# Kernel optimization log

Measured on AMD Instinct MI355X. Metric: run time of the kernel, lower is better.

The kernel has to match this reference:

```python
import jax, jax.numpy as jnp
import numpy as np
from jax import lax

B, T, H, IN = 1024, 100, 512, 4  # batch, seq len (fixed 100 in source), hidden, nucleotide dim


def _lstm_cell(x, h, c, Wih, Whh, b):
    # PyTorch gate order: i, f, g, o ; b = b_ih + b_hh
    gates = x @ Wih.T + h @ Whh.T + b
    i, f, g, o = jnp.split(gates, 4, axis=-1)
    c = jax.nn.sigmoid(f) * c + jax.nn.sigmoid(i) * jnp.tanh(g)
    h = jax.nn.sigmoid(o) * jnp.tanh(c)
    return h, c


def _run_layer(xs, Wih, Whh, b):
    # xs: [T, B, in] -> ys: [T, B, H], final (h, c)
    Bn = xs.shape[1]
    h0 = jnp.zeros((Bn, H), xs.dtype)
    c0 = jnp.zeros((Bn, H), xs.dtype)

    def step(carry, x):
        h, c = carry
        h, c = _lstm_cell(x, h, c, Wih, Whh, b)
        return (h, c), h

    (h, c), ys = lax.scan(step, (h0, c0), xs)
    return ys, h, c


def setup_inputs() -> dict:
    key = jax.random.key(0)
    ks = jax.random.split(key, 16)
    s = lambda fan: 1.0 / np.sqrt(fan)

    def W(k, shape, fan):
        return jax.random.uniform(k, shape, jnp.float32, -s(fan), s(fan))

    inp = {
        "X": jax.random.normal(ks[0], (B, T, IN), jnp.float32),
        "epoch": 10,
        # encoder LSTM (2 layers)
        "enc_Wih0": W(ks[1], (4 * H, IN), H),
        "enc_Whh0": W(ks[2], (4 * H, H), H),
        "enc_b0": jnp.zeros((4 * H,), jnp.float32),
        "enc_Wih1": W(ks[3], (4 * H, H), H),
        "enc_Whh1": W(ks[4], (4 * H, H), H),
        "enc_b1": jnp.zeros((4 * H,), jnp.float32),
        # decoder LSTM (2 layers, input dim = seq_in_dim = 4)
        "dec_Wih0": W(ks[5], (4 * H, IN), H),
        "dec_Whh0": W(ks[6], (4 * H, H), H),
        "dec_b0": jnp.zeros((4 * H,), jnp.float32),
        "dec_Wih1": W(ks[7], (4 * H, H), H),
        "dec_Whh1": W(ks[8], (4 * H, H), H),
        "dec_b1": jnp.zeros((4 * H,), jnp.float32),
        # predict_MLP = Linear(H, 4)
        "Wp": W(ks[9], (IN, H), H),
        "bp": jnp.zeros((IN,), jnp.float32),
    }
    return inp


def reference(X, epoch, enc_Wih0, enc_Whh0, enc_b0, enc_Wih1, enc_Whh1, enc_b1,
              dec_Wih0, dec_Whh0, dec_b0, dec_Wih1, dec_Whh1, dec_b1, Wp, bp):
    # ---- Encoder: 2-layer LSTM over X (batch_first -> scan over time) ----
    xs = jnp.swapaxes(X, 0, 1)  # [T, B, 4]
    ys0, h0e, c0e = _run_layer(xs, enc_Wih0, enc_Whh0, enc_b0)
    _, h1e, c1e = _run_layer(ys0, enc_Wih1, enc_Whh1, enc_b1)

    #      discretize_input=False) ----
    Bn = X.shape[0]
    x_init = jnp.zeros((Bn, IN), X.dtype)

    def dec_step(carry, _):
        x, h0, c0, h1, c1 = carry
        h0, c0 = _lstm_cell(x, h0, c0, dec_Wih0, dec_Whh0, dec_b0)
        h1, c1 = _lstm_cell(h0, h1, c1, dec_Wih1, dec_Whh1, dec_b1)
        pred = h1 @ Wp.T + bp                 # [B, 4] logits
        x_next = jax.nn.softmax(pred, axis=-1)
        return (x_next, h0, c0, h1, c1), pred

    _, preds = lax.scan(dec_step, (x_init, h0e, c0e, h1e, c1e), None, length=T)
    # out_seq list of [B,1,4] in torch -> stacked [B, 100, 4]
    return jnp.swapaxes(preds, 0, 1)
```

## Files before the change

kernel.cpp:

```cpp
#include <hip/hip_runtime.h>
#include <math.h>
#include <stdint.h>

typedef _Float16 f16;
typedef _Float16 f16x8 __attribute__((ext_vector_type(8)));
typedef float f32x16 __attribute__((ext_vector_type(16)));

#define BATCH 1024
#define HD    512
#define TST   100

__device__ __forceinline__ float4 coh_ld_x4(const void* p) {
    float4 v;
    asm volatile("global_load_dwordx4 %0, %1, off sc0 sc1" : "=v"(v) : "v"(p) : "memory");
    return v;
}
__device__ __forceinline__ float4 ld_x4(const void* p) {
    float4 v;
    asm volatile("global_load_dwordx4 %0, %1, off" : "=v"(v) : "v"(p) : "memory");
    return v;
}
__device__ __forceinline__ void coh_store_u32(uint32_t* p, uint32_t v) {
    asm volatile("global_store_dword %0, %1, off sc0 sc1" :: "v"(p), "v"(v) : "memory");
}
__device__ __forceinline__ void coh_store_i32(int* p, int v) {
    asm volatile("global_store_dword %0, %1, off sc0 sc1" :: "v"(p), "v"(v) : "memory");
}
__device__ __forceinline__ int coh_load_i32(const int* p) {
    int v;
    asm volatile("global_load_dword %0, %1, off sc0 sc1\n\ts_waitcnt vmcnt(0)"
                 : "=v"(v) : "v"(p) : "memory");
    return v;
}
__device__ __forceinline__ void drain_vm() {
    asm volatile("s_waitcnt vmcnt(0)" ::: "memory");
    __builtin_amdgcn_sched_barrier(0);
}
__device__ __forceinline__ void wait_vm(int n) {
    switch (n) {
    case 0:  asm volatile("s_waitcnt vmcnt(0)"  ::: "memory"); break;
    case 4:  asm volatile("s_waitcnt vmcnt(4)"  ::: "memory"); break;
    case 6:  asm volatile("s_waitcnt vmcnt(6)"  ::: "memory"); break;
    case 10: asm volatile("s_waitcnt vmcnt(10)" ::: "memory"); break;
    case 26: asm volatile("s_waitcnt vmcnt(26)" ::: "memory"); break;
    case 32: asm volatile("s_waitcnt vmcnt(32)" ::: "memory"); break;
    default: asm volatile("s_waitcnt vmcnt(34)" ::: "memory"); break;
    }
    __builtin_amdgcn_sched_barrier(0);
}

__device__ __forceinline__ float fast_sig(float x) {
    return 1.0f / (1.0f + __expf(-x));
}
__device__ __forceinline__ float fast_tanh(float x) {
    float xc = fminf(fmaxf(x, -15.0f), 15.0f);
    float e = __expf(2.0f * xc);
    return 1.0f - 2.0f / (e + 1.0f);
}

__global__ void split_w(const float* __restrict__ src0, int ksplit,
                        const float* __restrict__ src1, int NKT, f16* __restrict__ out)
{
    int c = blockIdx.x * 256 + threadIdx.x;
    int total = 8 * NKT * 4096;
    if (c >= total) return;
    int q = c & 4095;
    int t2 = c >> 12;
    int kt = t2 % NKT;
    int mt = t2 / NKT;
    int inner = q >> 8;
    int row = q & 255;
    int s = inner >> 2, p = (inner >> 1) & 1, half = inner & 1;
    int m = mt * 256 + row;
    int orow = (m & 3) * HD + (m >> 2);
    int kb = kt * 64 + s * 16 + half * 8;
    f16 v[8];
    #pragma unroll
    for (int e = 0; e < 8; ++e) {
        int k = kb + e;
        float w = (k < ksplit) ? src0[(size_t)orow * ksplit + k]
                               : src1[(size_t)orow * HD + (k - ksplit)];
        float w32 = w * 32.0f;
        f16 hi = (f16)w32;
        v[e] = p ? (f16)((w32 - (float)hi) * 2048.0f) : hi;
    }
    *(f16x8*)(out + (size_t)c * 8) = *(f16x8*)v;
}

__global__ void prep_b4(const float* __restrict__ b, float* __restrict__ bt) {
    int c = blockIdx.x * 256 + threadIdx.x;
    if (c < 2048) bt[c] = b[(c & 3) * HD + (c >> 2)];
}

__global__ void prep_wih4(const float* __restrict__ W, float* __restrict__ o) {
    int c = blockIdx.x * 256 + threadIdx.x;
    if (c < 8192) {
        int j = c & 3, g = (c >> 2) & 3, hl = c >> 4;
        o[c] = W[(size_t)(g * HD + hl) * 4 + j];
    }
}

__device__ __forceinline__ void publish(int* cell, int epoch) {
    drain_vm();
    __syncthreads();
    if (threadIdx.x == 0)
        coh_store_i32(cell, epoch);
}

__device__ __forceinline__ void wait2(const int* a, int ta, const int* b, int tb) {
    if (threadIdx.x < 64) {
        const int l = threadIdx.x & 7;
        const bool useB = (threadIdx.x & 8) != 0;
        const int* p = (useB ? b : a) + l * 16;
        const int tgt = useB ? tb : ta;
        for (;;) {
            int v = coh_load_i32(p);
            if (__all(v >= tgt)) break;
            __builtin_amdgcn_s_sleep(2);
        }
    }
    __syncthreads();
}

template<int NKT, bool RANK4>
__device__ __forceinline__ void layer_step(
    const f16* __restrict__ Wst, const f16* __restrict__ src1, const f16* __restrict__ src2,
    const float* __restrict__ wih4, const float* __restrict__ xin, int xstride,
    const float* __restrict__ bt4, float* __restrict__ cT, f16* __restrict__ hout,
    char* smem, int mt, int nt)
{
    const int tid  = threadIdx.x;
    const int lane = tid & 63;
    const int wv   = tid >> 6;
    const int col  = lane & 31;
    const int half = lane >> 5;
    const int xk   = lane & 15;
    const int n0   = nt * 32;

    const size_t tbaseA = (size_t)half * 4096 + (size_t)(wv * 64 + col) * 16;
    const int colb = col * 256;

    float4 ab0[4], ab1[4], ab2[4], ab3[4];
    float4 rb0[2], rb1[2];
    float4 xv = make_float4(0.f, 0.f, 0.f, 0.f);

    auto issueA = [&](int kt, int s, float4 (&bank)[4]) {
        const char* ga = (const char*)Wst + ((size_t)(mt * NKT + kt) << 16)
                       + ((size_t)s << 14) + tbaseA;
        bank[0] = ld_x4(ga);
        bank[1] = ld_x4(ga + 8192);
        bank[2] = ld_x4(ga + 512);
        bank[3] = ld_x4(ga + 8704);
    };
    auto issueB = [&](int kt, float4 (&rb)[2]) {
        #pragma unroll
        for (int i = 0; i < 2; ++i) {
            int u = i * 256 + tid;
            int bc = u >> 4, w16 = u & 15;
            int si = w16 ^ (bc & 15);
            int p = si >> 3;
            int kh = kt * 64 + ((si >> 1) & 3) * 16 + (si & 1) * 8;
            const f16* sp = src1; int kl = kh;
            if (NKT == 16 && kh >= 512) { sp = src2; kl = kh - 512; }
            rb[i] = coh_ld_x4(sp + (size_t)(n0 + bc) * 1024 + p * 512 + kl);
        }
    };

    f32x16 accA0 = {}, accA1 = {}, accB0 = {}, accB1 = {};

    if (RANK4) xv = coh_ld_x4(xin + (size_t)(n0 + col) * xstride);
    issueB(0, rb0);
    issueB(1, rb1);
    issueA(0, 0, ab0);
    issueA(0, 1, ab1);

    #pragma unroll
    for (int kt = 0; kt < NKT; ++kt) {
        char* buf = smem + (kt & 1) * 8192;
        wait_vm(kt == 0 ? 10 : kt == 1 ? 26 : kt == NKT - 1 ? 32 : 34);
        if ((kt & 1) == 0) {
            *(float4*)(buf + tid * 16)        = rb0[0];
            *(float4*)(buf + 4096 + tid * 16) = rb0[1];
            if (kt + 2 < NKT) issueB(kt + 2, rb0);
        } else {
            *(float4*)(buf + tid * 16)        = rb1[0];
            *(float4*)(buf + 4096 + tid * 16) = rb1[1];
            if (kt + 2 < NKT) issueB(kt + 2, rb1);
        }
        __syncthreads();

        #define KSTEP(S, BK)                                                              \
        {                                                                                 \
            f16x8 bh = *(const f16x8*)(buf + colb + ((((S) * 2 + half) ^ xk) << 4));       \
            f16x8 bl = *(const f16x8*)(buf + colb + (((8 + (S) * 2 + half) ^ xk) << 4));   \
            f16x8 ah0 = __builtin_bit_cast(f16x8, BK[0]);                                 \
            f16x8 al0 = __builtin_bit_cast(f16x8, BK[1]);                                 \
            f16x8 ah1 = __builtin_bit_cast(f16x8, BK[2]);                                 \
            f16x8 al1 = __builtin_bit_cast(f16x8, BK[3]);                                 \
            accA0 = __builtin_amdgcn_mfma_f32_32x32x16_f16(ah0, bh, accA0, 0, 0, 0);      \
            accB0 = __builtin_amdgcn_mfma_f32_32x32x16_f16(al0, bh, accB0, 0, 0, 0);      \
            accB0 = __builtin_amdgcn_mfma_f32_32x32x16_f16(ah0, bl, accB0, 0, 0, 0);      \
            accA1 = __builtin_amdgcn_mfma_f32_32x32x16_f16(ah1, bh, accA1, 0, 0, 0);      \
            accB1 = __builtin_amdgcn_mfma_f32_32x32x16_f16(al1, bh, accB1, 0, 0, 0);      \
            accB1 = __builtin_amdgcn_mfma_f32_32x32x16_f16(ah1, bl, accB1, 0, 0, 0);      \
        }

        wait_vm(kt >= NKT - 2 ? 4 : 6);
        KSTEP(0, ab0)
        issueA(kt, 2, ab2);
        wait_vm(kt >= NKT - 2 ? 4 : 6);
        KSTEP(1, ab1)
        issueA(kt, 3, ab3);
        wait_vm(4);
        KSTEP(2, ab2)
        if (kt + 1 < NKT) issueA(kt + 1, 0, ab0);
        wait_vm(kt == NKT - 1 ? 0 : 4);
        KSTEP(3, ab3)
        if (kt + 1 < NKT) issueA(kt + 1, 1, ab1);
        #undef KSTEP
    }

    const float sA = 1.0f / 1024.0f;
    const float sB = 1.0f / (1024.0f * 2048.0f);
    uint32_t* htile = (uint32_t*)(smem + 16384);

    #pragma unroll
    for (int f = 0; f < 2; ++f) {
        const f32x16 aA = f ? accA1 : accA0;
        const f32x16 aB = f ? accB1 : accB0;
        #pragma unroll
        for (int qq = 0; qq < 4; ++qq) {
            const int hl_loc = wv * 16 + f * 8 + 2 * qq + half;
            const int hl = mt * 64 + hl_loc;
            const float4 bv = *(const float4*)(bt4 + hl * 4);
            float g0 = aA[4 * qq + 0] * sA + aB[4 * qq + 0] * sB + bv.x;
            float g1 = aA[4 * qq + 1] * sA + aB[4 * qq + 1] * sB + bv.y;
            float g2 = aA[4 * qq + 2] * sA + aB[4 * qq + 2] * sB + bv.z;
            float g3 = aA[4 * qq + 3] * sA + aB[4 * qq + 3] * sB + bv.w;
            if (RANK4) {
                const float4* wr = (const float4*)(wih4 + hl * 16);
                g0 += wr[0].x * xv.x + wr[0].y * xv.y + wr[0].z * xv.z + wr[0].w * xv.w;
                g1 += wr[1].x * xv.x + wr[1].y * xv.y + wr[1].z * xv.z + wr[1].w * xv.w;
                g2 += wr[2].x * xv.x + wr[2].y * xv.y + wr[2].z * xv.z + wr[2].w * xv.w;
                g3 += wr[3].x * xv.x + wr[3].y * xv.y + wr[3].z * xv.z + wr[3].w * xv.w;
            }
            const int n = n0 + col;
            const size_t co = (size_t)hl * 1024 + n;
            const float cold = cT[co];
            const float si = fast_sig(g0);
            const float sf = fast_sig(g1);
            const float so = fast_sig(g3);
            const float cn = sf * cold + si * fast_tanh(g2);
            const float hn = so * fast_tanh(cn);
            cT[co] = cn;
            const float h32v = hn * 32.0f;
            const f16 hi = (f16)h32v;
            const f16 lo = (f16)((h32v - (float)hi) * 2048.0f);
            uint32_t pk = ((uint32_t)__builtin_bit_cast(uint16_t, lo) << 16)
                        | (uint32_t)__builtin_bit_cast(uint16_t, hi);
            htile[col * 65 + hl_loc] = pk;
        }
    }
    __syncthreads();
    uint32_t* h32out = (uint32_t*)hout;
    #pragma unroll
    for (int e = 0; e < 8; ++e) {
        int u = e * 256 + tid;
        int cc = u >> 6;
        int rem = u & 63;
        int pl = rem >> 5;
        int w = rem & 31;
        uint32_t t0 = htile[cc * 65 + 2 * w];
        uint32_t t1 = htile[cc * 65 + 2 * w + 1];
        uint32_t word = pl ? ((t1 & 0xffff0000u) | (t0 >> 16))
                           : ((t1 << 16) | (t0 & 0xffffu));
        coh_store_u32(h32out + (size_t)(n0 + cc) * 512 + pl * 256 + mt * 32 + w, word);
    }
}

__device__ __forceinline__ void pred_step(
    const f16* __restrict__ h1, const float* __restrict__ Wp, const float* __restrict__ bp,
    float* __restrict__ outp, float* __restrict__ xfb, int t, int mt, int nt)
{
    const int lane = threadIdx.x & 63;
    const int wv = threadIdx.x >> 6;
    const int n = nt * 32 + mt * 4 + wv;
    const f16* hr = h1 + (size_t)n * 1024;
    const int k0 = lane * 8;
    float4 hv4 = coh_ld_x4(hr + k0);
    float4 lv4 = coh_ld_x4(hr + 512 + k0);
    drain_vm();
    f16x8 hv = __builtin_bit_cast(f16x8, hv4);
    f16x8 lv = __builtin_bit_cast(f16x8, lv4);
    float h[8];
    #pragma unroll
    for (int e = 0; e < 8; ++e)
        h[e] = (float)hv[e] * 0.03125f + (float)lv[e] * (1.0f / 65536.0f);
    float a[4] = {};
    #pragma unroll
    for (int g = 0; g < 4; ++g) {
        const float4 wa = *(const float4*)(Wp + g * HD + k0);
        const float4 wb = *(const float4*)(Wp + g * HD + k0 + 4);
        a[g] = h[0]*wa.x + h[1]*wa.y + h[2]*wa.z + h[3]*wa.w
             + h[4]*wb.x + h[5]*wb.y + h[6]*wb.z + h[7]*wb.w;
    }
    #pragma unroll
    for (int off = 32; off > 0; off >>= 1) {
        a[0] += __shfl_xor(a[0], off);
        a[1] += __shfl_xor(a[1], off);
        a[2] += __shfl_xor(a[2], off);
        a[3] += __shfl_xor(a[3], off);
    }
    if (lane == 0) {
        const float4 bv = *(const float4*)bp;
        float v0 = a[0] + bv.x, v1 = a[1] + bv.y, v2 = a[2] + bv.z, v3 = a[3] + bv.w;
        float* op = outp + (size_t)n * (TST * 4) + t * 4;
        op[0] = v0; op[1] = v1; op[2] = v2; op[3] = v3;
        float m = fmaxf(fmaxf(v0, v1), fmaxf(v2, v3));
        float e0 = expf(v0 - m), e1 = expf(v1 - m), e2 = expf(v2 - m), e3 = expf(v3 - m);
        float inv = 1.0f / (e0 + e1 + e2 + e3);
        uint32_t* xp = (uint32_t*)(xfb + n * 4);
        float s0 = e0 * inv, s1 = e1 * inv, s2 = e2 * inv, s3 = e3 * inv;
        coh_store_u32(xp + 0, __builtin_bit_cast(uint32_t, s0));
        coh_store_u32(xp + 1, __builtin_bit_cast(uint32_t, s1));
        coh_store_u32(xp + 2, __builtin_bit_cast(uint32_t, s2));
        coh_store_u32(xp + 3, __builtin_bit_cast(uint32_t, s3));
    }
}

struct Params {
    const f16 *WE0, *WE1, *WD0, *WD1;
    const float *wih4E, *wih4D, *btE0, *btE1, *btD0, *btD1;
    const float *X, *Wp, *bp;
    f16 *h0a, *h0b, *h1a, *h1b;
    float *c0, *c1;
    float *xfb0, *xfb1;
    float *out;
    int *f0, *f1, *fp;
};

__launch_bounds__(256, 1) __global__ void lstm_persistent(Params P)
{
    __shared__ __align__(16) char smem[16384 + 8448];
    const int bx = blockIdx.x;
    const int mt = bx & 7;
    const int nt = bx >> 3;
    int* f0g = P.f0 + nt * 128;
    int* f1g = P.f1 + nt * 128;
    int* fpg = P.fp + nt * 128;
    int* my0 = f0g + mt * 16;
    int* my1 = f1g + mt * 16;
    int* myp = fpg + mt * 16;
    f16* h0b_[2] = { P.h0a, P.h0b };
    f16* h1b_[2] = { P.h1a, P.h1b };
    float* xfb_[2] = { P.xfb0, P.xfb1 };

    for (int u = 0; u < 2 * TST; ++u) {
        const bool enc = (u < TST);
        const int t = enc ? u : u - TST;

        if (enc) wait2(f0g, u, f0g, u);
        else     wait2(f0g, u, fpg, t);
        layer_step<8, true>(enc ? P.WE0 : P.WD0,
                            h0b_[(u + 1) & 1], nullptr,
                            enc ? P.wih4E : P.wih4D,
                            enc ? (P.X + t * 4) : xfb_[(t + 1) & 1],
                            enc ? (TST * 4) : 4,
                            enc ? P.btE0 : P.btD0,
                            P.c0, h0b_[u & 1], smem, mt, nt);
        publish(my0, u + 1);

        wait2(f0g, u + 1, f1g, u);
        layer_step<16, false>(enc ? P.WE1 : P.WD1,
                              h0b_[u & 1], h1b_[(u + 1) & 1],
                              nullptr, nullptr, 0,
                              enc ? P.btE1 : P.btD1,
                              P.c1, h1b_[u & 1], smem, mt, nt);
        publish(my1, u + 1);

        if (!enc) {
            wait2(f1g, u + 1, f1g, u + 1);
            pred_step(h1b_[u & 1], P.Wp, P.bp, P.out, xfb_[t & 1], t, mt, nt);
            publish(myp, t + 1);
        }
    }
}

extern "C" void kernel_launch(void* const* d_in, const int* in_sizes, int n_in,
                              void* d_out, int out_size, void* d_ws, size_t ws_size,
                              hipStream_t stream)
{
    const float* X     = (const float*)d_in[0];
    const float* eWih0 = (const float*)d_in[2];
    const float* eWhh0 = (const float*)d_in[3];
    const float* eb0   = (const float*)d_in[4];
    const float* eWih1 = (const float*)d_in[5];
    const float* eWhh1 = (const float*)d_in[6];
    const float* eb1   = (const float*)d_in[7];
    const float* dWih0 = (const float*)d_in[8];
    const float* dWhh0 = (const float*)d_in[9];
    const float* db0   = (const float*)d_in[10];
    const float* dWih1 = (const float*)d_in[11];
    const float* dWhh1 = (const float*)d_in[12];
    const float* db1   = (const float*)d_in[13];
    const float* Wp    = (const float*)d_in[14];
    const float* bp    = (const float*)d_in[15];

    char* ws = (char*)d_ws;
    size_t off = 0;
    auto alloc = [&](size_t bytes) { char* p = ws + off; off += (bytes + 255) & ~(size_t)255; return p; };
    f16* WE0 = (f16*)alloc((size_t)8 * 8  * 65536);
    f16* WE1 = (f16*)alloc((size_t)8 * 16 * 65536);
    f16* WD0 = (f16*)alloc((size_t)8 * 8  * 65536);
    f16* WD1 = (f16*)alloc((size_t)8 * 16 * 65536);
    float* wih4E = (float*)alloc(8192 * 4);
    float* wih4D = (float*)alloc(8192 * 4);
    float* btE0 = (float*)alloc(2048 * 4);
    float* btE1 = (float*)alloc(2048 * 4);
    float* btD0 = (float*)alloc(2048 * 4);
    float* btD1 = (float*)alloc(2048 * 4);
    f16* h0a = (f16*)alloc((size_t)BATCH * 1024 * 2);
    f16* h0b = (f16*)alloc((size_t)BATCH * 1024 * 2);
    f16* h1a = (f16*)alloc((size_t)BATCH * 1024 * 2);
    f16* h1b = (f16*)alloc((size_t)BATCH * 1024 * 2);
    float* c0  = (float*)alloc((size_t)HD * BATCH * 4);
    float* c1  = (float*)alloc((size_t)HD * BATCH * 4);
    float* xfb0 = (float*)alloc((size_t)BATCH * 4 * 4);
    float* xfb1 = (float*)alloc((size_t)BATCH * 4 * 4);
    int* f0 = (int*)alloc(32 * 128 * 4);
    int* f1 = (int*)alloc(32 * 128 * 4);
    int* fp = (int*)alloc(32 * 128 * 4);
    if (off > ws_size) return;

    split_w<<<(8 * 8  * 4096) / 256, 256, 0, stream>>>(nullptr, 0,   eWhh0, 8,  WE0);
    split_w<<<(8 * 16 * 4096) / 256, 256, 0, stream>>>(eWih1, 512, eWhh1, 16, WE1);
    split_w<<<(8 * 8  * 4096) / 256, 256, 0, stream>>>(nullptr, 0,   dWhh0, 8,  WD0);
    split_w<<<(8 * 16 * 4096) / 256, 256, 0, stream>>>(dWih1, 512, dWhh1, 16, WD1);
    prep_wih4<<<32, 256, 0, stream>>>(eWih0, wih4E);
    prep_wih4<<<32, 256, 0, stream>>>(dWih0, wih4D);
    prep_b4<<<8, 256, 0, stream>>>(eb0, btE0);
    prep_b4<<<8, 256, 0, stream>>>(eb1, btE1);
    prep_b4<<<8, 256, 0, stream>>>(db0, btD0);
    prep_b4<<<8, 256, 0, stream>>>(db1, btD1);

    hipMemsetAsync(h0b, 0, (size_t)BATCH * 1024 * 2, stream);
    hipMemsetAsync(h1b, 0, (size_t)BATCH * 1024 * 2, stream);
    hipMemsetAsync(c0, 0, (size_t)HD * BATCH * 4, stream);
    hipMemsetAsync(c1, 0, (size_t)HD * BATCH * 4, stream);
    hipMemsetAsync(xfb1, 0, (size_t)BATCH * 4 * 4, stream);
    hipMemsetAsync(f0, 0, 32 * 128 * 4, stream);
    hipMemsetAsync(f1, 0, 32 * 128 * 4, stream);
    hipMemsetAsync(fp, 0, 32 * 128 * 4, stream);

    Params P;
    P.WE0 = WE0; P.WE1 = WE1; P.WD0 = WD0; P.WD1 = WD1;
    P.wih4E = wih4E; P.wih4D = wih4D;
    P.btE0 = btE0; P.btE1 = btE1; P.btD0 = btD0; P.btD1 = btD1;
    P.X = X; P.Wp = Wp; P.bp = bp;
    P.h0a = h0a; P.h0b = h0b; P.h1a = h1a; P.h1b = h1b;
    P.c0 = c0; P.c1 = c1;
    P.xfb0 = xfb0; P.xfb1 = xfb1;
    P.out = (float*)d_out;
    P.f0 = f0; P.f1 = f1; P.fp = fp;

    lstm_persistent<<<256, 256, 0, stream>>>(P);

    (void)in_sizes; (void)n_in; (void)out_size;
}
```

Baseline: 7.458 ms.

## Enlarge persistent LSTM tiles to 128 hidden units by 64 batch with 512-thread blocks

Result: slower. 17.91 ms (+140.1%).

```diff
diff --git a/kernel.cpp b/kernel.cpp
--- a/kernel.cpp
+++ b/kernel.cpp
@@ -41,10 +41,8 @@
     case 0:  asm volatile("s_waitcnt vmcnt(0)"  ::: "memory"); break;
     case 4:  asm volatile("s_waitcnt vmcnt(4)"  ::: "memory"); break;
     case 6:  asm volatile("s_waitcnt vmcnt(6)"  ::: "memory"); break;
-    case 10: asm volatile("s_waitcnt vmcnt(10)" ::: "memory"); break;
-    case 26: asm volatile("s_waitcnt vmcnt(26)" ::: "memory"); break;
-    case 32: asm volatile("s_waitcnt vmcnt(32)" ::: "memory"); break;
-    default: asm volatile("s_waitcnt vmcnt(34)" ::: "memory"); break;
+    case 8:  asm volatile("s_waitcnt vmcnt(8)"  ::: "memory"); break;
+    default: asm volatile("s_waitcnt vmcnt(10)" ::: "memory"); break;
     }
     __builtin_amdgcn_sched_barrier(0);
 }
@@ -62,16 +60,16 @@
                         const float* __restrict__ src1, int NKT, f16* __restrict__ out)
 {
     int c = blockIdx.x * 256 + threadIdx.x;
-    int total = 8 * NKT * 4096;
+    int total = 4 * NKT * 8192;
     if (c >= total) return;
-    int q = c & 4095;
-    int t2 = c >> 12;
+    int u = c & 8191;
+    int t2 = c >> 13;
     int kt = t2 % NKT;
     int mt = t2 / NKT;
-    int inner = q >> 8;
-    int row = q & 255;
+    int inner = u >> 9;
+    int row = u & 511;
     int s = inner >> 2, p = (inner >> 1) & 1, half = inner & 1;
-    int m = mt * 256 + row;
+    int m = mt * 512 + row;
     int orow = (m & 3) * HD + (m >> 2);
     int kb = kt * 64 + s * 16 + half * 8;
     f16 v[8];
@@ -106,11 +104,10 @@
     if (threadIdx.x == 0)
         coh_store_i32(cell, epoch);
 }
-
 __device__ __forceinline__ void wait2(const int* a, int ta, const int* b, int tb) {
     if (threadIdx.x < 64) {
-        const int l = threadIdx.x & 7;
-        const bool useB = (threadIdx.x & 8) != 0;
+        const int l = threadIdx.x & 3;
+        const bool useB = (threadIdx.x & 4) != 0;
         const int* p = (useB ? b : a) + l * 16;
         const int tgt = useB ? tb : ta;
         for (;;) {
@@ -134,28 +131,26 @@
     const int wv   = tid >> 6;
     const int col  = lane & 31;
     const int half = lane >> 5;
-    const int xk   = lane & 15;
-    const int n0   = nt * 32;
-
-    const size_t tbaseA = (size_t)half * 4096 + (size_t)(wv * 64 + col) * 16;
-    const int colb = col * 256;
-
-    float4 ab0[4], ab1[4], ab2[4], ab3[4];
+    const int xk   = col & 15;
+    const int n0   = nt * 64;
+
+    const size_t tbaseA = (size_t)half * 8192 + (size_t)(wv * 64 + col) * 16;
+
+    float4 abk[4][4];
     float4 rb0[2], rb1[2];
-    float4 xv = make_float4(0.f, 0.f, 0.f, 0.f);
 
     auto issueA = [&](int kt, int s, float4 (&bank)[4]) {
-        const char* ga = (const char*)Wst + ((size_t)(mt * NKT + kt) << 16)
-                       + ((size_t)s << 14) + tbaseA;
+        const char* ga = (const char*)Wst + ((size_t)(mt * NKT + kt) << 17)
+                       + ((size_t)s << 15) + tbaseA;
         bank[0] = ld_x4(ga);
-        bank[1] = ld_x4(ga + 8192);
+        bank[1] = ld_x4(ga + 16384);
         bank[2] = ld_x4(ga + 512);
-        bank[3] = ld_x4(ga + 8704);
+        bank[3] = ld_x4(ga + 16384 + 512);
     };
     auto issueB = [&](int kt, float4 (&rb)[2]) {
         #pragma unroll
         for (int i = 0; i < 2; ++i) {
-            int u = i * 256 + tid;
+            int u = i * 512 + tid;
             int bc = u >> 4, w16 = u & 15;
             int si = w16 ^ (bc & 15);
             int p = si >> 3;
@@ -166,115 +161,130 @@
         }
     };
 
-    f32x16 accA0 = {}, accA1 = {}, accB0 = {}, accB1 = {};
-
-    if (RANK4) xv = coh_ld_x4(xin + (size_t)(n0 + col) * xstride);
+    f32x16 accA[2][2] = {};
+    f32x16 accB[2][2] = {};
+
     issueB(0, rb0);
     issueB(1, rb1);
-    issueA(0, 0, ab0);
-    issueA(0, 1, ab1);
+    issueA(0, 0, abk[0]);
+    issueA(0, 1, abk[1]);
 
     #pragma unroll
     for (int kt = 0; kt < NKT; ++kt) {
-        char* buf = smem + (kt & 1) * 8192;
-        wait_vm(kt == 0 ? 10 : kt == 1 ? 26 : kt == NKT - 1 ? 32 : 34);
+        char* buf = smem + (kt & 1) * 16384;
+        wait_vm(kt == NKT - 1 ? 8 : 10);
         if ((kt & 1) == 0) {
             *(float4*)(buf + tid * 16)        = rb0[0];
-            *(float4*)(buf + 4096 + tid * 16) = rb0[1];
-            if (kt + 2 < NKT) issueB(kt + 2, rb0);
+            *(float4*)(buf + 8192 + tid * 16) = rb0[1];
         } else {
             *(float4*)(buf + tid * 16)        = rb1[0];
-            *(float4*)(buf + 4096 + tid * 16) = rb1[1];
-            if (kt + 2 < NKT) issueB(kt + 2, rb1);
+            *(float4*)(buf + 8192 + tid * 16) = rb1[1];
         }
         __syncthreads();
 
-        #define KSTEP(S, BK)                                                              \
-        {                                                                                 \
-            f16x8 bh = *(const f16x8*)(buf + colb + ((((S) * 2 + half) ^ xk) << 4));       \
-            f16x8 bl = *(const f16x8*)(buf + colb + (((8 + (S) * 2 + half) ^ xk) << 4));   \
-            f16x8 ah0 = __builtin_bit_cast(f16x8, BK[0]);                                 \
-            f16x8 al0 = __builtin_bit_cast(f16x8, BK[1]);                                 \
-            f16x8 ah1 = __builtin_bit_cast(f16x8, BK[2]);                                 \
-            f16x8 al1 = __builtin_bit_cast(f16x8, BK[3]);                                 \
-            accA0 = __builtin_amdgcn_mfma_f32_32x32x16_f16(ah0, bh, accA0, 0, 0, 0);      \
-            accB0 = __builtin_amdgcn_mfma_f32_32x32x16_f16(al0, bh, accB0, 0, 0, 0);      \
-            accB0 = __builtin_amdgcn_mfma_f32_32x32x16_f16(ah0, bl, accB0, 0, 0, 0);      \
-            accA1 = __builtin_amdgcn_mfma_f32_32x32x16_f16(ah1, bh, accA1, 0, 0, 0);      \
-            accB1 = __builtin_amdgcn_mfma_f32_32x32x16_f16(al1, bh, accB1, 0, 0, 0);      \
-            accB1 = __builtin_amdgcn_mfma_f32_32x32x16_f16(ah1, bl, accB1, 0, 0, 0);      \
-        }
-
-        wait_vm(kt >= NKT - 2 ? 4 : 6);
-        KSTEP(0, ab0)
-        issueA(kt, 2, ab2);
-        wait_vm(kt >= NKT - 2 ? 4 : 6);
-        KSTEP(1, ab1)
-        issueA(kt, 3, ab3);
+        #define KSTEP(S, BK)                                                          \
+        {                                                                             \
+            f16x8 ah0 = __builtin_bit_cast(f16x8, BK[0]);                             \
+            f16x8 al0 = __builtin_bit_cast(f16x8, BK[1]);                             \
+            f16x8 ah1 = __builtin_bit_cast(f16x8, BK[2]);                             \
+            f16x8 al1 = __builtin_bit_cast(f16x8, BK[3]);                             \
+            _Pragma("unroll")                                                         \
+            for (int nf = 0; nf < 2; ++nf) {                                          \
+                const char* cb = buf + (nf * 32 + col) * 256;                         \
+                f16x8 bh = *(const f16x8*)(cb + ((((S) * 2 + half) ^ xk) << 4));      \
+                f16x8 bl = *(const f16x8*)(cb + (((8 + (S) * 2 + half) ^ xk) << 4));  \
+                accA[0][nf] = __builtin_amdgcn_mfma_f32_32x32x16_f16(ah0, bh, accA[0][nf], 0, 0, 0); \
+                accB[0][nf] = __builtin_amdgcn_mfma_f32_32x32x16_f16(al0, bh, accB[0][nf], 0, 0, 0); \
+                accB[0][nf] = __builtin_amdgcn_mfma_f32_32x32x16_f16(ah0, bl, accB[0][nf], 0, 0, 0); \
+                accA[1][nf] = __builtin_amdgcn_mfma_f32_32x32x16_f16(ah1, bh, accA[1][nf], 0, 0, 0); \
+                accB[1][nf] = __builtin_amdgcn_mfma_f32_32x32x16_f16(al1, bh, accB[1][nf], 0, 0, 0); \
+                accB[1][nf] = __builtin_amdgcn_mfma_f32_32x32x16_f16(ah1, bl, accB[1][nf], 0, 0, 0); \
+            }                                                                         \
+        }
+
+        const int w01 = (kt == 0 || kt == NKT - 1) ? 4 : 6;
+        wait_vm(w01);
+        KSTEP(0, abk[0])
+        issueA(kt, 2, abk[2]);
+        wait_vm(w01);
+        KSTEP(1, abk[1])
+        issueA(kt, 3, abk[3]);
         wait_vm(4);
-        KSTEP(2, ab2)
-        if (kt + 1 < NKT) issueA(kt + 1, 0, ab0);
+        KSTEP(2, abk[2])
+        if (kt + 1 < NKT) issueA(kt + 1, 0, abk[0]);
         wait_vm(kt == NKT - 1 ? 0 : 4);
-        KSTEP(3, ab3)
-        if (kt + 1 < NKT) issueA(kt + 1, 1, ab1);
+        KSTEP(3, abk[3])
+        if (kt + 1 < NKT) issueA(kt + 1, 1, abk[1]);
+        if (kt + 2 < NKT) {
+            if ((kt & 1) == 0) issueB(kt + 2, rb0);
+            else               issueB(kt + 2, rb1);
+        }
         #undef KSTEP
     }
 
     const float sA = 1.0f / 1024.0f;
     const float sB = 1.0f / (1024.0f * 2048.0f);
-    uint32_t* htile = (uint32_t*)(smem + 16384);
-
+    float4 xq[2];
+    if (RANK4) {
+        xq[0] = coh_ld_x4(xin + (size_t)(n0 + col) * xstride);
+        xq[1] = coh_ld_x4(xin + (size_t)(n0 + 32 + col) * xstride);
+        drain_vm();
+    }
+    uint32_t* htile = (uint32_t*)(smem + 32768);
     #pragma unroll
     for (int f = 0; f < 2; ++f) {
-        const f32x16 aA = f ? accA1 : accA0;
-        const f32x16 aB = f ? accB1 : accB0;
         #pragma unroll
         for (int qq = 0; qq < 4; ++qq) {
             const int hl_loc = wv * 16 + f * 8 + 2 * qq + half;
-            const int hl = mt * 64 + hl_loc;
+            const int hl = mt * 128 + hl_loc;
             const float4 bv = *(const float4*)(bt4 + hl * 4);
-            float g0 = aA[4 * qq + 0] * sA + aB[4 * qq + 0] * sB + bv.x;
-            float g1 = aA[4 * qq + 1] * sA + aB[4 * qq + 1] * sB + bv.y;
-            float g2 = aA[4 * qq + 2] * sA + aB[4 * qq + 2] * sB + bv.z;
-            float g3 = aA[4 * qq + 3] * sA + aB[4 * qq + 3] * sB + bv.w;
-            if (RANK4) {
-                const float4* wr = (const float4*)(wih4 + hl * 16);
-                g0 += wr[0].x * xv.x + wr[0].y * xv.y + wr[0].z * xv.z + wr[0].w * xv.w;
-                g1 += wr[1].x * xv.x + wr[1].y * xv.y + wr[1].z * xv.z + wr[1].w * xv.w;
-                g2 += wr[2].x * xv.x + wr[2].y * xv.y + wr[2].z * xv.z + wr[2].w * xv.w;
-                g3 += wr[3].x * xv.x + wr[3].y * xv.y + wr[3].z * xv.z + wr[3].w * xv.w;
+            #pragma unroll
+            for (int nf = 0; nf < 2; ++nf) {
+                const int col_loc = nf * 32 + col;
+                const int n = n0 + col_loc;
+                float g0 = accA[f][nf][4 * qq + 0] * sA + accB[f][nf][4 * qq + 0] * sB + bv.x;
+                float g1 = accA[f][nf][4 * qq + 1] * sA + accB[f][nf][4 * qq + 1] * sB + bv.y;
+                float g2 = accA[f][nf][4 * qq + 2] * sA + accB[f][nf][4 * qq + 2] * sB + bv.z;
+                float g3 = accA[f][nf][4 * qq + 3] * sA + accB[f][nf][4 * qq + 3] * sB + bv.w;
+                if (RANK4) {
+                    const float4* wr = (const float4*)(wih4 + hl * 16);
+                    const float4 x4 = xq[nf];
+                    g0 += wr[0].x * x4.x + wr[0].y * x4.y + wr[0].z * x4.z + wr[0].w * x4.w;
+                    g1 += wr[1].x * x4.x + wr[1].y * x4.y + wr[1].z * x4.z + wr[1].w * x4.w;
+                    g2 += wr[2].x * x4.x + wr[2].y * x4.y + wr[2].z * x4.z + wr[2].w * x4.w;
+                    g3 += wr[3].x * x4.x + wr[3].y * x4.y + wr[3].z * x4.z + wr[3].w * x4.w;
+                }
+                const size_t co = (size_t)hl * 1024 + n;
+                const float cold = cT[co];
+                const float si = fast_sig(g0);
+                const float sf = fast_sig(g1);
+                const float so = fast_sig(g3);
+                const float cn = sf * cold + si * fast_tanh(g2);
+                const float hn = so * fast_tanh(cn);
+                cT[co] = cn;
+                const float h32v = hn * 32.0f;
+                const f16 hi = (f16)h32v;
+                const f16 lo = (f16)((h32v - (float)hi) * 2048.0f);
+                uint32_t pk = ((uint32_t)__builtin_bit_cast(uint16_t, lo) << 16)
+                            | (uint32_t)__builtin_bit_cast(uint16_t, hi);
+                htile[col_loc * 129 + hl_loc] = pk;
             }
-            const int n = n0 + col;
-            const size_t co = (size_t)hl * 1024 + n;
-            const float cold = cT[co];
-            const float si = fast_sig(g0);
-            const float sf = fast_sig(g1);
-            const float so = fast_sig(g3);
-            const float cn = sf * cold + si * fast_tanh(g2);
-            const float hn = so * fast_tanh(cn);
-            cT[co] = cn;
-            const float h32v = hn * 32.0f;
-            const f16 hi = (f16)h32v;
-            const f16 lo = (f16)((h32v - (float)hi) * 2048.0f);
-            uint32_t pk = ((uint32_t)__builtin_bit_cast(uint16_t, lo) << 16)
-                        | (uint32_t)__builtin_bit_cast(uint16_t, hi);
-            htile[col * 65 + hl_loc] = pk;
         }
     }
     __syncthreads();
     uint32_t* h32out = (uint32_t*)hout;
     #pragma unroll
-    for (int e = 0; e < 8; ++e) {
-        int u = e * 256 + tid;
-        int cc = u >> 6;
-        int rem = u & 63;
-        int pl = rem >> 5;
-        int w = rem & 31;
-        uint32_t t0 = htile[cc * 65 + 2 * w];
-        uint32_t t1 = htile[cc * 65 + 2 * w + 1];
+    for (int e = 0; e < 16; ++e) {
+        int u = e * 512 + tid;
+        int cc = u >> 7;
+        int rem = u & 127;
+        int pl = rem >> 6;
+        int w = rem & 63;
+        uint32_t t0 = htile[cc * 129 + 2 * w];
+        uint32_t t1 = htile[cc * 129 + 2 * w + 1];
         uint32_t word = pl ? ((t1 & 0xffff0000u) | (t0 >> 16))
                            : ((t1 << 16) | (t0 & 0xffffu));
-        coh_store_u32(h32out + (size_t)(n0 + cc) * 512 + pl * 256 + mt * 32 + w, word);
+        coh_store_u32(h32out + (size_t)(n0 + cc) * 512 + pl * 256 + mt * 64 + w, word);
     }
 }
 
@@ -284,47 +294,50 @@
 {
     const int lane = threadIdx.x & 63;
     const int wv = threadIdx.x >> 6;
-    const int n = nt * 32 + mt * 4 + wv;
-    const f16* hr = h1 + (size_t)n * 1024;
-    const int k0 = lane * 8;
-    float4 hv4 = coh_ld_x4(hr + k0);
-    float4 lv4 = coh_ld_x4(hr + 512 + k0);
-    drain_vm();
-    f16x8 hv = __builtin_bit_cast(f16x8, hv4);
-    f16x8 lv = __builtin_bit_cast(f16x8, lv4);
-    float h[8];
     #pragma unroll
-    for (int e = 0; e < 8; ++e)
-        h[e] = (float)hv[e] * 0.03125f + (float)lv[e] * (1.0f / 65536.0f);
-    float a[4] = {};
-    #pragma unroll
-    for (int g = 0; g < 4; ++g) {
-        const float4 wa = *(const float4*)(Wp + g * HD + k0);
-        const float4 wb = *(const float4*)(Wp + g * HD + k0 + 4);
-        a[g] = h[0]*wa.x + h[1]*wa.y + h[2]*wa.z + h[3]*wa.w
-             + h[4]*wb.x + h[5]*wb.y + h[6]*wb.z + h[7]*wb.w;
-    }
-    #pragma unroll
-    for (int off = 32; off > 0; off >>= 1) {
-        a[0] += __shfl_xor(a[0], off);
-        a[1] += __shfl_xor(a[1], off);
-        a[2] += __shfl_xor(a[2], off);
-        a[3] += __shfl_xor(a[3], off);
-    }
-    if (lane == 0) {
-        const float4 bv = *(const float4*)bp;
-        float v0 = a[0] + bv.x, v1 = a[1] + bv.y, v2 = a[2] + bv.z, v3 = a[3] + bv.w;
-        float* op = outp + (size_t)n * (TST * 4) + t * 4;
-        op[0] = v0; op[1] = v1; op[2] = v2; op[3] = v3;
-        float m = fmaxf(fmaxf(v0, v1), fmaxf(v2, v3));
-        float e0 = expf(v0 - m), e1 = expf(v1 - m), e2 = expf(v2 - m), e3 = expf(v3 - m);
-        float inv = 1.0f / (e0 + e1 + e2 + e3);
-        uint32_t* xp = (uint32_t*)(xfb + n * 4);
-        float s0 = e0 * inv, s1 = e1 * inv, s2 = e2 * inv, s3 = e3 * inv;
-        coh_store_u32(xp + 0, __builtin_bit_cast(uint32_t, s0));
-        coh_store_u32(xp + 1, __builtin_bit_cast(uint32_t, s1));
-        coh_store_u32(xp + 2, __builtin_bit_cast(uint32_t, s2));
-        coh_store_u32(xp + 3, __builtin_bit_cast(uint32_t, s3));
+    for (int it = 0; it < 2; ++it) {
+        const int n = nt * 64 + mt * 16 + it * 8 + wv;
+        const f16* hr = h1 + (size_t)n * 1024;
+        const int k0 = lane * 8;
+        float4 hv4 = coh_ld_x4(hr + k0);
+        float4 lv4 = coh_ld_x4(hr + 512 + k0);
+        drain_vm();
+        f16x8 hv = __builtin_bit_cast(f16x8, hv4);
+        f16x8 lv = __builtin_bit_cast(f16x8, lv4);
+        float h[8];
+        #pragma unroll
+        for (int e = 0; e < 8; ++e)
+            h[e] = (float)hv[e] * 0.03125f + (float)lv[e] * (1.0f / 65536.0f);
+        float a[4] = {};
+        #pragma unroll
+        for (int g = 0; g < 4; ++g) {
+            const float4 wa = *(const float4*)(Wp + g * HD + k0);
+            const float4 wb = *(const float4*)(Wp + g * HD + k0 + 4);
+            a[g] = h[0]*wa.x + h[1]*wa.y + h[2]*wa.z + h[3]*wa.w
+                 + h[4]*wb.x + h[5]*wb.y + h[6]*wb.z + h[7]*wb.w;
+        }
+        #pragma unroll
+        for (int off = 32; off > 0; off >>= 1) {
+            a[0] += __shfl_xor(a[0], off);
+            a[1] += __shfl_xor(a[1], off);
+            a[2] += __shfl_xor(a[2], off);
+            a[3] += __shfl_xor(a[3], off);
+        }
+        if (lane == 0) {
+            const float4 bv = *(const float4*)bp;
+            float v0 = a[0] + bv.x, v1 = a[1] + bv.y, v2 = a[2] + bv.z, v3 = a[3] + bv.w;
+            float* op = outp + (size_t)n * (TST * 4) + t * 4;
+            op[0] = v0; op[1] = v1; op[2] = v2; op[3] = v3;
+            float m = fmaxf(fmaxf(v0, v1), fmaxf(v2, v3));
+            float e0 = expf(v0 - m), e1 = expf(v1 - m), e2 = expf(v2 - m), e3 = expf(v3 - m);
+            float inv = 1.0f / (e0 + e1 + e2 + e3);
+            uint32_t* xp = (uint32_t*)(xfb + n * 4);
+            float s0 = e0 * inv, s1 = e1 * inv, s2 = e2 * inv, s3 = e3 * inv;
+            coh_store_u32(xp + 0, __builtin_bit_cast(uint32_t, s0));
+            coh_store_u32(xp + 1, __builtin_bit_cast(uint32_t, s1));
+            coh_store_u32(xp + 2, __builtin_bit_cast(uint32_t, s2));
+            coh_store_u32(xp + 3, __builtin_bit_cast(uint32_t, s3));
+        }
     }
 }
 
@@ -339,15 +352,15 @@
     int *f0, *f1, *fp;
 };
 
-__launch_bounds__(256, 1) __global__ void lstm_persistent(Params P)
+__launch_bounds__(512, 1) __global__ void lstm_persistent(Params P)
 {
-    __shared__ __align__(16) char smem[16384 + 8448];
+    __shared__ __align__(16) char smem[32768 + 33024];
     const int bx = blockIdx.x;
-    const int mt = bx & 7;
-    const int nt = bx >> 3;
-    int* f0g = P.f0 + nt * 128;
-    int* f1g = P.f1 + nt * 128;
-    int* fpg = P.fp + nt * 128;
+    const int mt = bx & 3;
+    const int nt = bx >> 2;
+    int* f0g = P.f0 + nt * 64;
+    int* f1g = P.f1 + nt * 64;
+    int* fpg = P.fp + nt * 64;
     int* my0 = f0g + mt * 16;
     int* my1 = f1g + mt * 16;
     int* myp = fpg + mt * 16;
@@ -409,10 +422,10 @@
     char* ws = (char*)d_ws;
     size_t off = 0;
     auto alloc = [&](size_t bytes) { char* p = ws + off; off += (bytes + 255) & ~(size_t)255; return p; };
-    f16* WE0 = (f16*)alloc((size_t)8 * 8  * 65536);
-    f16* WE1 = (f16*)alloc((size_t)8 * 16 * 65536);
-    f16* WD0 = (f16*)alloc((size_t)8 * 8  * 65536);
-    f16* WD1 = (f16*)alloc((size_t)8 * 16 * 65536);
+    f16* WE0 = (f16*)alloc((size_t)4 * 8  * 131072);
+    f16* WE1 = (f16*)alloc((size_t)4 * 16 * 131072);
+    f16* WD0 = (f16*)alloc((size_t)4 * 8  * 131072);
+    f16* WD1 = (f16*)alloc((size_t)4 * 16 * 131072);
     float* wih4E = (float*)alloc(8192 * 4);
     float* wih4D = (float*)alloc(8192 * 4);
     float* btE0 = (float*)alloc(2048 * 4);
@@ -427,15 +440,15 @@
     float* c1  = (float*)alloc((size_t)HD * BATCH * 4);
     float* xfb0 = (float*)alloc((size_t)BATCH * 4 * 4);
     float* xfb1 = (float*)alloc((size_t)BATCH * 4 * 4);
-    int* f0 = (int*)alloc(32 * 128 * 4);
-    int* f1 = (int*)alloc(32 * 128 * 4);
-    int* fp = (int*)alloc(32 * 128 * 4);
+    int* f0 = (int*)alloc(16 * 64 * 4);
+    int* f1 = (int*)alloc(16 * 64 * 4);
+    int* fp = (int*)alloc(16 * 64 * 4);
     if (off > ws_size) return;
 
-    split_w<<<(8 * 8  * 4096) / 256, 256, 0, stream>>>(nullptr, 0,   eWhh0, 8,  WE0);
-    split_w<<<(8 * 16 * 4096) / 256, 256, 0, stream>>>(eWih1, 512, eWhh1, 16, WE1);
-    split_w<<<(8 * 8  * 4096) / 256, 256, 0, stream>>>(nullptr, 0,   dWhh0, 8,  WD0);
-    split_w<<<(8 * 16 * 4096) / 256, 256, 0, stream>>>(dWih1, 512, dWhh1, 16, WD1);
+    split_w<<<(4 * 8  * 8192) / 256, 256, 0, stream>>>(nullptr, 0,   eWhh0, 8,  WE0);
+    split_w<<<(4 * 16 * 8192) / 256, 256, 0, stream>>>(eWih1, 512, eWhh1, 16, WE1);
+    split_w<<<(4 * 8  * 8192) / 256, 256, 0, stream>>>(nullptr, 0,   dWhh0, 8,  WD0);
+    split_w<<<(4 * 16 * 8192) / 256, 256, 0, stream>>>(dWih1, 512, dWhh1, 16, WD1);
     prep_wih4<<<32, 256, 0, stream>>>(eWih0, wih4E);
     prep_wih4<<<32, 256, 0, stream>>>(dWih0, wih4D);
     prep_b4<<<8, 256, 0, stream>>>(eb0, btE0);
@@ -448,9 +461,9 @@
     hipMemsetAsync(c0, 0, (size_t)HD * BATCH * 4, stream);
     hipMemsetAsync(c1, 0, (size_t)HD * BATCH * 4, stream);
     hipMemsetAsync(xfb1, 0, (size_t)BATCH * 4 * 4, stream);
-    hipMemsetAsync(f0, 0, 32 * 128 * 4, stream);
-    hipMemsetAsync(f1, 0, 32 * 128 * 4, stream);
-    hipMemsetAsync(fp, 0, 32 * 128 * 4, stream);
+    hipMemsetAsync(f0, 0, 16 * 64 * 4, stream);
+    hipMemsetAsync(f1, 0, 16 * 64 * 4, stream);
+    hipMemsetAsync(fp, 0, 16 * 64 * 4, stream);
 
     Params P;
     P.WE0 = WE0; P.WE1 = WE1; P.WD0 = WD0; P.WD1 = WD1;
@@ -463,7 +476,7 @@
     P.out = (float*)d_out;
     P.f0 = f0; P.f1 = f1; P.fp = fp;
 
-    lstm_persistent<<<256, 256, 0, stream>>>(P);
+    lstm_persistent<<<64, 512, 0, stream>>>(P);
 
     (void)in_sizes; (void)n_in; (void)out_size;
 }
```
